# Kernel optimization log

Measured on AMD Instinct MI355X. Metric: run time of the kernel, lower is better.

The kernel has to match this reference:

```python
import jax, jax.numpy as jnp
import numpy as np

K = 2  # number of propagation hops (SGConv K)
NEG_SLOPE = 0.1


def setup_inputs() -> dict:
    key = jax.random.key(0)
    k1, k2, k3, k4 = jax.random.split(key, 4)
    N, E, C_in, C_out = 50000, 800000, 128, 512
    x = jax.random.normal(k1, (N, C_in), dtype=jnp.float32)
    edge_index = jax.random.randint(k2, (2, E), 0, N, dtype=jnp.int64)
    W = jax.random.normal(k3, (C_out, C_in), dtype=jnp.float32) * (1.0 / np.sqrt(C_in))
    b = jax.random.normal(k4, (C_out,), dtype=jnp.float32) * 0.01
    return {"x": x, "edge_index": edge_index, "W": W, "b": b}


def reference(x, edge_index, W, b):
    N = x.shape[0]
    # gcn_norm with self-loops (PyG SGConv default: add_self_loops=True)
    loop = jnp.arange(N, dtype=edge_index.dtype)
    src = jnp.concatenate([edge_index[0], loop])  # message sources j
    dst = jnp.concatenate([edge_index[1], loop])  # aggregation targets i
    deg = jax.ops.segment_sum(jnp.ones_like(dst, dtype=x.dtype), dst, num_segments=N)
    dinv = jnp.where(deg > 0, jax.lax.rsqrt(deg), 0.0)
    norm = dinv[src] * dinv[dst]  # [E+N]
    h = x
    for _ in range(K):
        h = jax.ops.segment_sum(norm[:, None] * h[src], dst, num_segments=N)
    y = h @ W.T + b
    return jnp.where(y >= 0, y, NEG_SLOPE * y)  # LeakyReLU(0.1)
```

## Files before the change

### kernel.cpp

```cpp
#include <hip/hip_runtime.h>
#include <hip/hip_bf16.h>

#define CIN 128
#define COUT 512
#define NEG_SLOPE 0.1f

typedef __bf16 bf16x8 __attribute__((ext_vector_type(8)));
typedef float f32x4 __attribute__((ext_vector_type(4)));

static __device__ __forceinline__ unsigned short f2bf(float f) {
  unsigned int u = __builtin_bit_cast(unsigned int, f);
  unsigned int lsb = (u >> 16) & 1u;
  u += 0x7fffu + lsb;
  return (unsigned short)(u >> 16);
}
static __device__ __forceinline__ float bf_lo(unsigned int u) {
  return __builtin_bit_cast(float, u << 16);
}
static __device__ __forceinline__ float bf_hi(unsigned int u) {
  return __builtin_bit_cast(float, u & 0xffff0000u);
}
static __device__ __forceinline__ unsigned int pack2(float lo, float hi) {
  return (unsigned int)f2bf(lo) | ((unsigned int)f2bf(hi) << 16);
}

__global__ void detect_kernel(const int* __restrict__ raw, int* __restrict__ flag, int E) {
  __shared__ int any_nonzero;
  int tid = threadIdx.x;
  if (tid == 0) any_nonzero = 0;
  __syncthreads();
  int v1 = raw[2 * tid + 1];
  int v2 = raw[2 * (E / 2) + 2 * tid + 1];
  if (v1 != 0 || v2 != 0) atomicOr(&any_nonzero, 1);
  __syncthreads();
  if (tid == 0) *flag = any_nonzero ? 0 : 1;
}

__global__ void decode_count_kernel(const int* __restrict__ raw, const int* __restrict__ flag,
                                    int* __restrict__ srcA, int* __restrict__ dstA,
                                    int* __restrict__ rank, int* __restrict__ cnt,
                                    int E, int N) {
  int e = blockIdx.x * blockDim.x + threadIdx.x;
  if (e >= E) return;
  int is64 = *flag;
  int s, d;
  if (is64) {
    int2 sv = ((const int2*)raw)[e];
    int2 dv = ((const int2*)raw)[E + e];
    s = sv.x;
    d = dv.x;
  } else {
    s = raw[e];
    d = raw[E + e];
  }
  if ((unsigned)s >= (unsigned)N) s = 0;
  if ((unsigned)d >= (unsigned)N) d = 0;
  srcA[e] = s;
  dstA[e] = d;
  rank[e] = atomicAdd(&cnt[d], 1);
}

__global__ __launch_bounds__(256) void prep_kernel(const float* __restrict__ x,
                                                   const int* __restrict__ cnt,
                                                   unsigned short* __restrict__ xs,
                                                   const float* __restrict__ W,
                                                   unsigned short* __restrict__ Wbf, int N) {
  int idx = blockIdx.x * blockDim.x + threadIdx.x;
  int nx = N * (CIN / 4);
  if (idx < nx) {
    int row = idx >> 5;
    float d = 1.0f / sqrtf((float)(cnt[row] + 1));
    float4 v = ((const float4*)x)[idx];
    ushort4 o;
    o.x = f2bf(v.x * d); o.y = f2bf(v.y * d); o.z = f2bf(v.z * d); o.w = f2bf(v.w * d);
    ((ushort4*)xs)[idx] = o;
  } else {
    int i = idx - nx;
    if (i < (COUT * CIN / 4)) {
      float4 v = ((const float4*)W)[i];
      ushort4 o;
      o.x = f2bf(v.x); o.y = f2bf(v.y); o.z = f2bf(v.z); o.w = f2bf(v.w);
      ((ushort4*)Wbf)[i] = o;
    }
  }
}

__global__ __launch_bounds__(256) void scan1_kernel(const int* __restrict__ cnt,
                                                    int* __restrict__ rowptr,
                                                    int* __restrict__ bsum, int N) {
  __shared__ int buf[256];
  int tid = threadIdx.x;
  int base = blockIdx.x * 1024 + tid * 4;
  int v[4];
  int tot = 0;
#pragma unroll
  for (int k = 0; k < 4; ++k) {
    int i = base + k;
    v[k] = (i < N) ? cnt[i] : 0;
    tot += v[k];
  }
  buf[tid] = tot;
  __syncthreads();
  for (int off = 1; off < 256; off <<= 1) {
    int t = (tid >= off) ? buf[tid - off] : 0;
    __syncthreads();
    buf[tid] += t;
    __syncthreads();
  }
  int run = buf[tid] - tot;
  if (tid == 255) bsum[blockIdx.x] = buf[255];
#pragma unroll
  for (int k = 0; k < 4; ++k) {
    int i = base + k;
    if (i < N) rowptr[i] = run;
    run += v[k];
  }
}

__global__ void scan2_kernel(int* __restrict__ bsum, int nb) {
  __shared__ int buf[256];
  int tid = threadIdx.x;
  int v = (tid < nb) ? bsum[tid] : 0;
  buf[tid] = v;
  __syncthreads();
  for (int off = 1; off < 256; off <<= 1) {
    int t = (tid >= off) ? buf[tid - off] : 0;
    __syncthreads();
    buf[tid] += t;
    __syncthreads();
  }
  if (tid < nb) bsum[tid] = buf[tid] - v;
}

__global__ void scatter_kernel(const int* __restrict__ srcA, const int* __restrict__ dstA,
                               const int* __restrict__ rank, const int* __restrict__ rowptr,
                               const int* __restrict__ bsum, int* __restrict__ col, int E) {
  int e = blockIdx.x * blockDim.x + threadIdx.x;
  if (e < E) {
    int d = dstA[e];
    col[rowptr[d] + bsum[d >> 10] + rank[e]] = srcA[e];
  }
}

template <bool SQ>
__global__ __launch_bounds__(256) void hop_kernel(
    const unsigned short* __restrict__ Xs,
    const int* __restrict__ rowptr, const int* __restrict__ cnt,
    const int* __restrict__ bsum,
    const int* __restrict__ col, unsigned short* __restrict__ Y, int N) {
  int lane = threadIdx.x & 63;
  int wid = threadIdx.x >> 6;
  int node = blockIdx.x * 4 + wid;
  if (node >= N) return;
  int sub = lane & 15;
  int grp = lane >> 4;
  int beg = rowptr[node] + bsum[node >> 10];
  int num = cnt[node];
  const uint4* X4 = (const uint4*)Xs;
  float acc[8] = {0.f, 0.f, 0.f, 0.f, 0.f, 0.f, 0.f, 0.f};
  if (grp == 0) {
    uint4 s = X4[(size_t)node * 16 + sub];
    acc[0] = bf_lo(s.x); acc[1] = bf_hi(s.x);
    acc[2] = bf_lo(s.y); acc[3] = bf_hi(s.y);
    acc[4] = bf_lo(s.z); acc[5] = bf_hi(s.z);
    acc[6] = bf_lo(s.w); acc[7] = bf_hi(s.w);
  }
  const int* cp = col + beg;
  int kb = 0;
  for (; kb + 16 <= num; kb += 16) {
    int j0 = cp[kb + grp];
    int j1 = cp[kb + 4 + grp];
    int j2 = cp[kb + 8 + grp];
    int j3 = cp[kb + 12 + grp];
    uint4 v0 = X4[(size_t)j0 * 16 + sub];
    uint4 v1 = X4[(size_t)j1 * 16 + sub];
    uint4 v2 = X4[(size_t)j2 * 16 + sub];
    uint4 v3 = X4[(size_t)j3 * 16 + sub];
    acc[0] += bf_lo(v0.x); acc[1] += bf_hi(v0.x);
    acc[2] += bf_lo(v0.y); acc[3] += bf_hi(v0.y);
    acc[4] += bf_lo(v0.z); acc[5] += bf_hi(v0.z);
    acc[6] += bf_lo(v0.w); acc[7] += bf_hi(v0.w);
    acc[0] += bf_lo(v1.x); acc[1] += bf_hi(v1.x);
    acc[2] += bf_lo(v1.y); acc[3] += bf_hi(v1.y);
    acc[4] += bf_lo(v1.z); acc[5] += bf_hi(v1.z);
    acc[6] += bf_lo(v1.w); acc[7] += bf_hi(v1.w);
    acc[0] += bf_lo(v2.x); acc[1] += bf_hi(v2.x);
    acc[2] += bf_lo(v2.y); acc[3] += bf_hi(v2.y);
    acc[4] += bf_lo(v2.z); acc[5] += bf_hi(v2.z);
    acc[6] += bf_lo(v2.w); acc[7] += bf_hi(v2.w);
    acc[0] += bf_lo(v3.x); acc[1] += bf_hi(v3.x);
    acc[2] += bf_lo(v3.y); acc[3] += bf_hi(v3.y);
    acc[4] += bf_lo(v3.z); acc[5] += bf_hi(v3.z);
    acc[6] += bf_lo(v3.w); acc[7] += bf_hi(v3.w);
  }
  for (; kb < num; kb += 4) {
    int k = kb + grp;
    if (k < num) {
      int j0 = cp[k];
      uint4 v0 = X4[(size_t)j0 * 16 + sub];
      acc[0] += bf_lo(v0.x); acc[1] += bf_hi(v0.x);
      acc[2] += bf_lo(v0.y); acc[3] += bf_hi(v0.y);
      acc[4] += bf_lo(v0.z); acc[5] += bf_hi(v0.z);
      acc[6] += bf_lo(v0.w); acc[7] += bf_hi(v0.w);
    }
  }
#pragma unroll
  for (int r = 0; r < 8; ++r) acc[r] += __shfl_xor(acc[r], 16, 64);
#pragma unroll
  for (int r = 0; r < 8; ++r) acc[r] += __shfl_xor(acc[r], 32, 64);
  if (grp == 0) {
    float di = 1.0f / sqrtf((float)(num + 1));
    float sc = SQ ? di * di : di;
    uint4 o;
    o.x = pack2(acc[0] * sc, acc[1] * sc);
    o.y = pack2(acc[2] * sc, acc[3] * sc);
    o.z = pack2(acc[4] * sc, acc[5] * sc);
    o.w = pack2(acc[6] * sc, acc[7] * sc);
    ((uint4*)Y)[(size_t)node * 16 + sub] = o;
  }
}

__global__ __launch_bounds__(256) void gemm_kernel(
    const unsigned short* __restrict__ Abf, const unsigned short* __restrict__ Wbf,
    const float* __restrict__ bias, float* __restrict__ out, int M) {
  __shared__ float tile[16 * 516];
  int wave = threadIdx.x >> 6;
  int lane = threadIdx.x & 63;
  int quad = lane >> 4;
  int l16 = lane & 15;
  int mbase = blockIdx.x * 32;

  int m0 = mbase + l16;
  int m1 = mbase + 16 + l16;
  bool v0 = m0 < M;
  bool v1 = m1 < M;

  bf16x8 af[2][4];
#pragma unroll
  for (int kk = 0; kk < 4; ++kk) {
    af[0][kk] = v0 ? *(const bf16x8*)(Abf + (size_t)m0 * CIN + kk * 32 + quad * 8) : bf16x8{};
    af[1][kk] = v1 ? *(const bf16x8*)(Abf + (size_t)m1 * CIN + kk * 32 + quad * 8) : bf16x8{};
  }

  int nbase = wave * 128;
  f32x4 acc0[8], acc1[8];
#pragma unroll
  for (int nt = 0; nt < 8; ++nt) {
    int nrow = nbase + nt * 16 + l16;
    bf16x8 wf[4];
#pragma unroll
    for (int kk = 0; kk < 4; ++kk)
      wf[kk] = *(const bf16x8*)(Wbf + (size_t)nrow * CIN + kk * 32 + quad * 8);
    f32x4 a0 = {}, a1 = {};
#pragma unroll
    for (int kk = 0; kk < 4; ++kk) {
      a0 = __builtin_amdgcn_mfma_f32_16x16x32_bf16(wf[kk], af[0][kk], a0, 0, 0, 0);
      a1 = __builtin_amdgcn_mfma_f32_16x16x32_bf16(wf[kk], af[1][kk], a1, 0, 0, 0);
    }
    acc0[nt] = a0;
    acc1[nt] = a1;
  }

#pragma unroll
  for (int half = 0; half < 2; ++half) {
    if (half) __syncthreads();
#pragma unroll
    for (int nt = 0; nt < 8; ++nt) {
      int n0 = nbase + nt * 16 + quad * 4;
      float4 bv = *(const float4*)(bias + n0);
      f32x4 a = half ? acc1[nt] : acc0[nt];
      float4 o;
      o.x = a[0] + bv.x; o.x = (o.x >= 0.f) ? o.x : NEG_SLOPE * o.x;
      o.y = a[1] + bv.y; o.y = (o.y >= 0.f) ? o.y : NEG_SLOPE * o.y;
      o.z = a[2] + bv.z; o.z = (o.z >= 0.f) ? o.z : NEG_SLOPE * o.z;
      o.w = a[3] + bv.w; o.w = (o.w >= 0.f) ? o.w : NEG_SLOPE * o.w;
      *(float4*)&tile[l16 * 516 + n0] = o;
    }
    __syncthreads();
#pragma unroll
    for (int it = 0; it < 8; ++it) {
      int r = it * 2 + (threadIdx.x >> 7);
      int c = (threadIdx.x & 127) * 4;
      int m = mbase + half * 16 + r;
      if (m < M) *(float4*)(out + (size_t)m * COUT + c) = *(const float4*)&tile[r * 516 + c];
    }
  }
}

static inline size_t align_up(size_t v, size_t a) { return (v + a - 1) & ~(a - 1); }

extern "C" void kernel_launch(void* const* d_in, const int* in_sizes, int n_in,
                              void* d_out, int out_size, void* d_ws, size_t ws_size,
                              hipStream_t stream) {
  const float* x = (const float*)d_in[0];
  const int* edge_raw = (const int*)d_in[1];
  const float* W = (const float*)d_in[2];
  const float* b = (const float*)d_in[3];
  float* out = (float*)d_out;

  const int N = in_sizes[0] / CIN;
  const int E = in_sizes[1] / 2;
  const int NB = (N + 1023) / 1024;

  char* w = (char*)d_ws;
  int* flag = (int*)w;            w += align_up(sizeof(int), 256);
  int* bsum = (int*)w;            w += align_up(256 * 4, 256);
  int* cnt = (int*)w;             w += align_up((size_t)N * 4, 256);
  int* rowptr = (int*)w;          w += align_up((size_t)N * 4, 256);
  int* srcA = (int*)w;            w += align_up((size_t)E * 4, 256);
  int* dstA = (int*)w;            w += align_up((size_t)E * 4, 256);
  int* rank = (int*)w;            w += align_up((size_t)E * 4, 256);
  int* col = (int*)w;             w += align_up((size_t)E * 4, 256);
  unsigned short* h2bf = (unsigned short*)w;  w += align_up((size_t)N * CIN * 2, 256);
  unsigned short* Wbf = (unsigned short*)w;   w += align_up((size_t)COUT * CIN * 2, 256);

  size_t outb = (size_t)out_size * sizeof(float);
  size_t rowb = (size_t)N * CIN * sizeof(unsigned short);
  unsigned short* h1s = (unsigned short*)((char*)d_out + (outb - rowb));
  unsigned short* xs = (unsigned short*)((char*)d_out + (outb - 2 * rowb));

  hipMemsetAsync(cnt, 0, (size_t)N * sizeof(int), stream);

  detect_kernel<<<1, 64, 0, stream>>>(edge_raw, flag, E);
  decode_count_kernel<<<(E + 255) / 256, 256, 0, stream>>>(edge_raw, flag, srcA, dstA, rank, cnt, E, N);
  scan1_kernel<<<NB, 256, 0, stream>>>(cnt, rowptr, bsum, N);
  scan2_kernel<<<1, 256, 0, stream>>>(bsum, NB);
  scatter_kernel<<<(E + 255) / 256, 256, 0, stream>>>(srcA, dstA, rank, rowptr, bsum, col, E);
  prep_kernel<<<(N * (CIN / 4) + COUT * CIN / 4 + 255) / 256, 256, 0, stream>>>(x, cnt, xs, W, Wbf, N);

  hop_kernel<true><<<(N + 3) / 4, 256, 0, stream>>>(xs, rowptr, cnt, bsum, col, h1s, N);
  hop_kernel<false><<<(N + 3) / 4, 256, 0, stream>>>(h1s, rowptr, cnt, bsum, col, h2bf, N);

  gemm_kernel<<<(N + 31) / 32, 256, 0, stream>>>(h2bf, Wbf, b, out, N);
}
```

Measured before the change: 287.3 us.

## Fuse graph preprocessing kernels and widen hop-kernel tail handling

The separate format-detect kernel is folded into decode_count, which now checks per block whether the edge input uses 32- or 64-bit indices. The two-level prefix scan is replaced by a single scan whose blocks reserve their output base with an atomic counter. The scatter into CSR is fused with the bf16 conversion of x and W, and a single memset clears both the counter and the degree array. Together these cut the number of kernel launches and the serial dependencies between them. The hop kernel's one-neighbour-per-group tail loop is replaced by unrolled blocks of 8 and 4 plus a final partial step, to raise memory-level parallelism for low-degree nodes. Row segments are no longer laid out in node order, and the per-block index-format probe relies on the input values.

```diff
diff --git a/kernel.cpp b/kernel.cpp
--- a/kernel.cpp
+++ b/kernel.cpp
@@ -24,27 +24,21 @@
   return (unsigned int)f2bf(lo) | ((unsigned int)f2bf(hi) << 16);
 }
 
-__global__ void detect_kernel(const int* __restrict__ raw, int* __restrict__ flag, int E) {
-  __shared__ int any_nonzero;
-  int tid = threadIdx.x;
-  if (tid == 0) any_nonzero = 0;
-  __syncthreads();
-  int v1 = raw[2 * tid + 1];
-  int v2 = raw[2 * (E / 2) + 2 * tid + 1];
-  if (v1 != 0 || v2 != 0) atomicOr(&any_nonzero, 1);
-  __syncthreads();
-  if (tid == 0) *flag = any_nonzero ? 0 : 1;
-}
-
-__global__ void decode_count_kernel(const int* __restrict__ raw, const int* __restrict__ flag,
+__global__ void decode_count_kernel(const int* __restrict__ raw,
                                     int* __restrict__ srcA, int* __restrict__ dstA,
                                     int* __restrict__ rank, int* __restrict__ cnt,
                                     int E, int N) {
+  __shared__ int s_is32;
+  if (threadIdx.x == 0) s_is32 = 0;
+  __syncthreads();
   int e = blockIdx.x * blockDim.x + threadIdx.x;
+  int probe = 0;
+  if (e < E) probe = raw[2 * e + 1];
+  if (probe != 0) s_is32 = 1;
+  __syncthreads();
   if (e >= E) return;
-  int is64 = *flag;
   int s, d;
-  if (is64) {
+  if (!s_is32) {
     int2 sv = ((const int2*)raw)[e];
     int2 dv = ((const int2*)raw)[E + e];
     s = sv.x;
@@ -60,12 +54,52 @@
   rank[e] = atomicAdd(&cnt[d], 1);
 }
 
-__global__ __launch_bounds__(256) void prep_kernel(const float* __restrict__ x,
-                                                   const int* __restrict__ cnt,
-                                                   unsigned short* __restrict__ xs,
-                                                   const float* __restrict__ W,
-                                                   unsigned short* __restrict__ Wbf, int N) {
+__global__ __launch_bounds__(256) void scan_kernel(const int* __restrict__ cnt,
+                                                   int* __restrict__ rowptr,
+                                                   int* __restrict__ gcur, int N) {
+  __shared__ int buf[256];
+  __shared__ int sbase;
+  int tid = threadIdx.x;
+  int base = blockIdx.x * 1024 + tid * 4;
+  int v[4];
+  int tot = 0;
+#pragma unroll
+  for (int k = 0; k < 4; ++k) {
+    int i = base + k;
+    v[k] = (i < N) ? cnt[i] : 0;
+    tot += v[k];
+  }
+  buf[tid] = tot;
+  __syncthreads();
+  for (int off = 1; off < 256; off <<= 1) {
+    int t = (tid >= off) ? buf[tid - off] : 0;
+    __syncthreads();
+    buf[tid] += t;
+    __syncthreads();
+  }
+  if (tid == 255) sbase = atomicAdd(gcur, buf[255]);
+  __syncthreads();
+  int run = sbase + buf[tid] - tot;
+#pragma unroll
+  for (int k = 0; k < 4; ++k) {
+    int i = base + k;
+    if (i < N) rowptr[i] = run;
+    run += v[k];
+  }
+}
+
+__global__ __launch_bounds__(256) void scatter_prep_kernel(
+    const int* __restrict__ srcA, const int* __restrict__ dstA,
+    const int* __restrict__ rank, const int* __restrict__ rowptr,
+    int* __restrict__ col, int E,
+    const float* __restrict__ x, const int* __restrict__ cnt,
+    unsigned short* __restrict__ xs,
+    const float* __restrict__ W, unsigned short* __restrict__ Wbf, int N) {
   int idx = blockIdx.x * blockDim.x + threadIdx.x;
+  if (idx < E) {
+    int d = dstA[idx];
+    col[rowptr[d] + rank[idx]] = srcA[idx];
+  }
   int nx = N * (CIN / 4);
   if (idx < nx) {
     int row = idx >> 5;
@@ -85,68 +119,10 @@
   }
 }
 
-__global__ __launch_bounds__(256) void scan1_kernel(const int* __restrict__ cnt,
-                                                    int* __restrict__ rowptr,
-                                                    int* __restrict__ bsum, int N) {
-  __shared__ int buf[256];
-  int tid = threadIdx.x;
-  int base = blockIdx.x * 1024 + tid * 4;
-  int v[4];
-  int tot = 0;
-#pragma unroll
-  for (int k = 0; k < 4; ++k) {
-    int i = base + k;
-    v[k] = (i < N) ? cnt[i] : 0;
-    tot += v[k];
-  }
-  buf[tid] = tot;
-  __syncthreads();
-  for (int off = 1; off < 256; off <<= 1) {
-    int t = (tid >= off) ? buf[tid - off] : 0;
-    __syncthreads();
-    buf[tid] += t;
-    __syncthreads();
-  }
-  int run = buf[tid] - tot;
-  if (tid == 255) bsum[blockIdx.x] = buf[255];
-#pragma unroll
-  for (int k = 0; k < 4; ++k) {
-    int i = base + k;
-    if (i < N) rowptr[i] = run;
-    run += v[k];
-  }
-}
-
-__global__ void scan2_kernel(int* __restrict__ bsum, int nb) {
-  __shared__ int buf[256];
-  int tid = threadIdx.x;
-  int v = (tid < nb) ? bsum[tid] : 0;
-  buf[tid] = v;
-  __syncthreads();
-  for (int off = 1; off < 256; off <<= 1) {
-    int t = (tid >= off) ? buf[tid - off] : 0;
-    __syncthreads();
-    buf[tid] += t;
-    __syncthreads();
-  }
-  if (tid < nb) bsum[tid] = buf[tid] - v;
-}
-
-__global__ void scatter_kernel(const int* __restrict__ srcA, const int* __restrict__ dstA,
-                               const int* __restrict__ rank, const int* __restrict__ rowptr,
-                               const int* __restrict__ bsum, int* __restrict__ col, int E) {
-  int e = blockIdx.x * blockDim.x + threadIdx.x;
-  if (e < E) {
-    int d = dstA[e];
-    col[rowptr[d] + bsum[d >> 10] + rank[e]] = srcA[e];
-  }
-}
-
 template <bool SQ>
 __global__ __launch_bounds__(256) void hop_kernel(
     const unsigned short* __restrict__ Xs,
     const int* __restrict__ rowptr, const int* __restrict__ cnt,
-    const int* __restrict__ bsum,
     const int* __restrict__ col, unsigned short* __restrict__ Y, int N) {
   int lane = threadIdx.x & 63;
   int wid = threadIdx.x >> 6;
@@ -154,7 +130,7 @@
   if (node >= N) return;
   int sub = lane & 15;
   int grp = lane >> 4;
-  int beg = rowptr[node] + bsum[node >> 10];
+  int beg = rowptr[node];
   int num = cnt[node];
   const uint4* X4 = (const uint4*)Xs;
   float acc[8] = {0.f, 0.f, 0.f, 0.f, 0.f, 0.f, 0.f, 0.f};
@@ -193,16 +169,38 @@
     acc[4] += bf_lo(v3.z); acc[5] += bf_hi(v3.z);
     acc[6] += bf_lo(v3.w); acc[7] += bf_hi(v3.w);
   }
-  for (; kb < num; kb += 4) {
-    int k = kb + grp;
-    if (k < num) {
-      int j0 = cp[k];
-      uint4 v0 = X4[(size_t)j0 * 16 + sub];
-      acc[0] += bf_lo(v0.x); acc[1] += bf_hi(v0.x);
-      acc[2] += bf_lo(v0.y); acc[3] += bf_hi(v0.y);
-      acc[4] += bf_lo(v0.z); acc[5] += bf_hi(v0.z);
-      acc[6] += bf_lo(v0.w); acc[7] += bf_hi(v0.w);
-    }
+  int rem = num - kb;
+  if (rem >= 8) {
+    int j0 = cp[kb + grp];
+    int j1 = cp[kb + 4 + grp];
+    uint4 v0 = X4[(size_t)j0 * 16 + sub];
+    uint4 v1 = X4[(size_t)j1 * 16 + sub];
+    acc[0] += bf_lo(v0.x); acc[1] += bf_hi(v0.x);
+    acc[2] += bf_lo(v0.y); acc[3] += bf_hi(v0.y);
+    acc[4] += bf_lo(v0.z); acc[5] += bf_hi(v0.z);
+    acc[6] += bf_lo(v0.w); acc[7] += bf_hi(v0.w);
+    acc[0] += bf_lo(v1.x); acc[1] += bf_hi(v1.x);
+    acc[2] += bf_lo(v1.y); acc[3] += bf_hi(v1.y);
+    acc[4] += bf_lo(v1.z); acc[5] += bf_hi(v1.z);
+    acc[6] += bf_lo(v1.w); acc[7] += bf_hi(v1.w);
+    kb += 8; rem -= 8;
+  }
+  if (rem >= 4) {
+    int j0 = cp[kb + grp];
+    uint4 v0 = X4[(size_t)j0 * 16 + sub];
+    acc[0] += bf_lo(v0.x); acc[1] += bf_hi(v0.x);
+    acc[2] += bf_lo(v0.y); acc[3] += bf_hi(v0.y);
+    acc[4] += bf_lo(v0.z); acc[5] += bf_hi(v0.z);
+    acc[6] += bf_lo(v0.w); acc[7] += bf_hi(v0.w);
+    kb += 4; rem -= 4;
+  }
+  if (grp < rem) {
+    int j0 = cp[kb + grp];
+    uint4 v0 = X4[(size_t)j0 * 16 + sub];
+    acc[0] += bf_lo(v0.x); acc[1] += bf_hi(v0.x);
+    acc[2] += bf_lo(v0.y); acc[3] += bf_hi(v0.y);
+    acc[4] += bf_lo(v0.z); acc[5] += bf_hi(v0.z);
+    acc[6] += bf_lo(v0.w); acc[7] += bf_hi(v0.w);
   }
 #pragma unroll
   for (int r = 0; r < 8; ++r) acc[r] += __shfl_xor(acc[r], 16, 64);
@@ -303,8 +301,7 @@
   const int NB = (N + 1023) / 1024;
 
   char* w = (char*)d_ws;
-  int* flag = (int*)w;            w += align_up(sizeof(int), 256);
-  int* bsum = (int*)w;            w += align_up(256 * 4, 256);
+  int* gcur = (int*)w;            w += 256;
   int* cnt = (int*)w;             w += align_up((size_t)N * 4, 256);
   int* rowptr = (int*)w;          w += align_up((size_t)N * 4, 256);
   int* srcA = (int*)w;            w += align_up((size_t)E * 4, 256);
@@ -319,17 +316,18 @@
   unsigned short* h1s = (unsigned short*)((char*)d_out + (outb - rowb));
   unsigned short* xs = (unsigned short*)((char*)d_out + (outb - 2 * rowb));
 
-  hipMemsetAsync(cnt, 0, (size_t)N * sizeof(int), stream);
-
-  detect_kernel<<<1, 64, 0, stream>>>(edge_raw, flag, E);
-  decode_count_kernel<<<(E + 255) / 256, 256, 0, stream>>>(edge_raw, flag, srcA, dstA, rank, cnt, E, N);
-  scan1_kernel<<<NB, 256, 0, stream>>>(cnt, rowptr, bsum, N);
-  scan2_kernel<<<1, 256, 0, stream>>>(bsum, NB);
-  scatter_kernel<<<(E + 255) / 256, 256, 0, stream>>>(srcA, dstA, rank, rowptr, bsum, col, E);
-  prep_kernel<<<(N * (CIN / 4) + COUT * CIN / 4 + 255) / 256, 256, 0, stream>>>(x, cnt, xs, W, Wbf, N);
-
-  hop_kernel<true><<<(N + 3) / 4, 256, 0, stream>>>(xs, rowptr, cnt, bsum, col, h1s, N);
-  hop_kernel<false><<<(N + 3) / 4, 256, 0, stream>>>(h1s, rowptr, cnt, bsum, col, h2bf, N);
+  hipMemsetAsync(gcur, 0, 256 + (size_t)N * sizeof(int), stream);
+
+  decode_count_kernel<<<(E + 255) / 256, 256, 0, stream>>>(edge_raw, srcA, dstA, rank, cnt, E, N);
+  scan_kernel<<<NB, 256, 0, stream>>>(cnt, rowptr, gcur, N);
+
+  int prep_elems = N * (CIN / 4) + COUT * CIN / 4;
+  int sp_threads = (E > prep_elems) ? E : prep_elems;
+  scatter_prep_kernel<<<(sp_threads + 255) / 256, 256, 0, stream>>>(
+      srcA, dstA, rank, rowptr, col, E, x, cnt, xs, W, Wbf, N);
+
+  hop_kernel<true><<<(N + 3) / 4, 256, 0, stream>>>(xs, rowptr, cnt, col, h1s, N);
+  hop_kernel<false><<<(N + 3) / 4, 256, 0, stream>>>(h1s, rowptr, cnt, col, h2bf, N);
 
   gemm_kernel<<<(N + 31) / 32, 256, 0, stream>>>(h2bf, Wbf, b, out, N);
 }
```

Measured after the change: 284.3 us. About the same (-1.1%).
